# Optimization experiments

Hardware: AMD Instinct MI355X
Metric: run time of the kernel (lower is better)

Reference implementation:

```python
import jax, jax.numpy as jnp
import numpy as np

B, C, D_IN, E = 4000, 128, 9, 10          # nodes, channels, sum irrep dims (0e+1o+2e), elements
OUT_IRREPS = [(1, 8, 3), (3, 11, 4)]       # (d_out, k3 paths, k2 paths) for 0e and 1o; k1 = 1


def _sparse(key, shape, p=0.15):
    # mimic the sparse generalized Clebsch-Gordan (U-matrix) bases from e3nn
    k1, k2 = jax.random.split(key)
    vals = jax.random.normal(k1, shape, dtype=jnp.float32)
    mask = (jax.random.uniform(k2, shape) < p).astype(jnp.float32)
    return vals * mask


def setup_inputs() -> dict:
    key = jax.random.key(0)
    ks = jax.random.split(key, 20)
    x = jax.random.normal(ks[0], (B, C, D_IN), dtype=jnp.float32)
    elems = jax.random.randint(ks[1], (B,), 0, E)
    attrs = jax.nn.one_hot(elems, E, dtype=jnp.float32)  # one-hot element embedding
    inp = {"x": x, "attrs": attrs}
    i = 2
    for n, (d, k3, k2) in enumerate(OUT_IRREPS):
        inp[f"U3_{n}"] = _sparse(ks[i], (d, D_IN, D_IN, D_IN, k3)); i += 1
        inp[f"U2_{n}"] = _sparse(ks[i], (d, D_IN, D_IN, k2)); i += 1
        inp[f"U1_{n}"] = _sparse(ks[i], (d, D_IN, 1)); i += 1
        inp[f"W3_{n}"] = jax.random.normal(ks[i], (E, k3, C), dtype=jnp.float32) / k3; i += 1
        inp[f"W2_{n}"] = jax.random.normal(ks[i], (E, k2, C), dtype=jnp.float32) / k2; i += 1
        inp[f"W1_{n}"] = jax.random.normal(ks[i], (E, 1, C), dtype=jnp.float32); i += 1
    return inp


def _contract(x, attrs, U3, U2, U1, W3, W2, W1):
    # MACE Contraction.forward: highest correlation order, then recursive descent
    # out = einsum('...ik,ekc,bci,be->bc...', U3, W3, x, attrs)  expressed efficiently:
    w3 = jnp.einsum("ekc,be->bkc", W3, attrs)                 # per-node element-selected weights
    out = jnp.einsum("dijpk,bkc,bcp->bcdij", U3, w3, x)       # [b,c,d,i,j]
    w2 = jnp.einsum("ekc,be->bkc", W2, attrs)
    c2 = jnp.einsum("dijk,bkc->bcdij", U2, w2) + out
    out = jnp.einsum("bcdij,bcj->bcdi", c2, x)                # contract one index with x
    w1 = jnp.einsum("ekc,be->bkc", W1, attrs)
    c1 = jnp.einsum("dik,bkc->bcdi", U1, w1) + out
    out = jnp.einsum("bcdi,bci->bcd", c1, x)                  # [b,c,d_out]
    return out.reshape(out.shape[0], -1)                      # [b, c*d_out]


def reference(x, attrs, U3_0, U2_0, U1_0, W3_0, W2_0, W1_0,
              U3_1, U2_1, U1_1, W3_1, W2_1, W1_1):
    o0 = _contract(x, attrs, U3_0, U2_0, U1_0, W3_0, W2_0, W1_0)  # 0e output: [b, 128]
    o1 = _contract(x, attrs, U3_1, U2_1, U1_1, W3_1, W2_1, W1_1)  # 1o output: [b, 384]
    return jnp.concatenate([o0, o1], axis=-1)                     # [b, 512]
```

## Files before the change

kernel.cpp:

```cpp
#include <hip/hip_runtime.h>

#define B_NODES 4000
#define C_CH    128
#define E_ELEM  10
#define NT1 9
#define NT2 45
#define NT3 165
#define NT  219
#define DG  4


#define OFF_A3_0 0
#define OFF_A3_1 1320
#define OFF_A2_0 6765
#define OFF_A2_1 6900
#define OFF_A1_0 7440
#define OFF_A1_1 7449
#define A_TOTAL  7476
#define OFF_G_BYTES 32768

__device__ inline void decode3(int t, int& i, int& j, int& p) {
    int idx = 0;
    for (int a = 0; a < 9; a++)
        for (int b = a; b < 9; b++)
            for (int c = b; c < 9; c++) {
                if (idx == t) { i = a; j = b; p = c; return; }
                idx++;
            }
}

__device__ inline void decode2(int t, int& i, int& j) {
    int idx = 0;
    for (int a = 0; a < 9; a++)
        for (int b = a; b < 9; b++) {
            if (idx == t) { i = a; j = b; return; }
            idx++;
        }
}

__device__ inline float sum3(const float* U, int d, int K, int k, int i, int j, int p) {
    auto at = [&](int a, int b, int c) {
        return U[(((d * 9 + a) * 9 + b) * 9 + c) * K + k];
    };
    if (i == j && j == p) return at(i, i, i);
    if (i == j)           return at(i, i, p) + at(i, p, i) + at(p, i, i);
    if (j == p)           return at(i, j, j) + at(j, i, j) + at(j, j, i);
    return at(i, j, p) + at(i, p, j) + at(j, i, p) + at(j, p, i) + at(p, i, j) + at(p, j, i);
}

__device__ inline float sum2(const float* U, int d, int K, int k, int i, int j) {
    auto at = [&](int a, int b) { return U[((d * 9 + a) * 9 + b) * K + k]; };
    return (i == j) ? at(i, i) : (at(i, j) + at(j, i));
}

__device__ inline unsigned short f2bf(float f) {
    unsigned u = __float_as_uint(f);
    unsigned r = u + 0x7fffu + ((u >> 16) & 1u);
    return (unsigned short)(r >> 16);
}

__global__ void a_build(const float* __restrict__ U3_0, const float* __restrict__ U2_0,
                        const float* __restrict__ U1_0, const float* __restrict__ U3_1,
                        const float* __restrict__ U2_1, const float* __restrict__ U1_1,
                        float* __restrict__ ws) {
    int tid = blockIdx.x * blockDim.x + threadIdx.x;
    if (tid < 1320) {
        int t3 = tid / 8, k = tid % 8;
        int i, j, p; decode3(t3, i, j, p);
        ws[OFF_A3_0 + tid] = sum3(U3_0, 0, 8, k, i, j, p);
    } else if (tid < 1320 + 5445) {
        int r = tid - 1320;
        int d = r / (165 * 11); int r2 = r % (165 * 11);
        int t3 = r2 / 11, k = r2 % 11;
        int i, j, p; decode3(t3, i, j, p);
        ws[OFF_A3_1 + r] = sum3(U3_1, d, 11, k, i, j, p);
    } else if (tid < 6765 + 135) {
        int r = tid - 6765;
        int t2 = r / 3, k = r % 3;
        int i, j; decode2(t2, i, j);
        ws[OFF_A2_0 + r] = sum2(U2_0, 0, 3, k, i, j);
    } else if (tid < 6900 + 540) {
        int r = tid - 6900;
        int d = r / 180; int t2 = (r % 180) / 4; int k = r % 4;
        int i, j; decode2(t2, i, j);
        ws[OFF_A2_1 + r] = sum2(U2_1, d, 4, k, i, j);
    } else if (tid < 7440 + 9) {
        int i = tid - 7440;
        ws[OFF_A1_0 + i] = U1_0[i];
    } else if (tid < 7449 + 27) {
        int r = tid - 7449;
        ws[OFF_A1_1 + r] = U1_1[r];
    }
}

__global__ void g_build(const float* __restrict__ W3_0, const float* __restrict__ W2_0,
                        const float* __restrict__ W1_0, const float* __restrict__ W3_1,
                        const float* __restrict__ W2_1, const float* __restrict__ W1_1,
                        const float* __restrict__ ws, unsigned short* __restrict__ G) {
    int tid = blockIdx.x * blockDim.x + threadIdx.x;
    if (tid >= E_ELEM * NT * C_CH) return;
    int c = tid & (C_CH - 1);
    int r = tid >> 7;
    int t = r % NT;
    int e = r / NT;

    float g[4];
    if (t < NT1) {
        int i = t;
        float w0 = W1_0[e * C_CH + c];
        float w1 = W1_1[e * C_CH + c];
        g[0] = ws[OFF_A1_0 + i] * w0;
        for (int d = 0; d < 3; d++) g[1 + d] = ws[OFF_A1_1 + d * 9 + i] * w1;
    } else if (t < NT1 + NT2) {
        int t2 = t - NT1;
        float s = 0.f;
        for (int k = 0; k < 3; k++) s += ws[OFF_A2_0 + t2 * 3 + k] * W2_0[(e * 3 + k) * C_CH + c];
        g[0] = s;
        for (int d = 0; d < 3; d++) {
            s = 0.f;
            for (int k = 0; k < 4; k++) s += ws[OFF_A2_1 + (d * 45 + t2) * 4 + k] * W2_1[(e * 4 + k) * C_CH + c];
            g[1 + d] = s;
        }
    } else {
        int t3 = t - NT1 - NT2;
        float s = 0.f;
        for (int k = 0; k < 8; k++) s += ws[OFF_A3_0 + t3 * 8 + k] * W3_0[(e * 8 + k) * C_CH + c];
        g[0] = s;
        for (int d = 0; d < 3; d++) {
            s = 0.f;
            for (int k = 0; k < 11; k++) s += ws[OFF_A3_1 + (d * 165 + t3) * 11 + k] * W3_1[(e * 11 + k) * C_CH + c];
            g[1 + d] = s;
        }
    }
    uint2 u;
    u.x = (unsigned)f2bf(g[0]) | ((unsigned)f2bf(g[1]) << 16);
    u.y = (unsigned)f2bf(g[2]) | ((unsigned)f2bf(g[3]) << 16);
    reinterpret_cast<uint2*>(G)[tid] = u;
}

__global__ void __launch_bounds__(C_CH) sc_main(const float* __restrict__ x,
                                                const float* __restrict__ attrs,
                                                const unsigned short* __restrict__ G,
                                                float* __restrict__ out) {
    int b = blockIdx.x;
    int c = threadIdx.x;

    int e = 0;
#pragma unroll
    for (int q = 0; q < E_ELEM; q++) e += (attrs[b * E_ELEM + q] > 0.5f) ? q : 0;

    float y[9];
#pragma unroll
    for (int i = 0; i < 9; i++) y[i] = x[(b * C_CH + c) * 9 + i];

    float d2[45];
    {
        int q = 0;
#pragma unroll
        for (int i = 0; i < 9; i++)
#pragma unroll
            for (int j = i; j < 9; j++) { d2[q] = y[i] * y[j]; q++; }
    }

    const uint2* gp = reinterpret_cast<const uint2*>(G) + (e * NT * C_CH + c);
    float a0 = 0.f, a1 = 0.f, a2 = 0.f, a3 = 0.f;

#define FMA4(U, PHI)                                                        \
    do {                                                                    \
        float _p = (PHI);                                                   \
        a0 = fmaf(_p, __uint_as_float((U).x << 16), a0);                    \
        a1 = fmaf(_p, __uint_as_float((U).x & 0xffff0000u), a1);            \
        a2 = fmaf(_p, __uint_as_float((U).y << 16), a2);                    \
        a3 = fmaf(_p, __uint_as_float((U).y & 0xffff0000u), a3);            \
    } while (0)

    int t = 0;
#pragma unroll
    for (int i = 0; i < 9; i++) {
        uint2 u = gp[t * C_CH]; t++;
        FMA4(u, y[i]);
    }
    {
        int q = 0;
#pragma unroll
        for (int i = 0; i < 9; i++)
#pragma unroll
            for (int j = i; j < 9; j++) {
                uint2 u = gp[t * C_CH]; t++;
                FMA4(u, d2[q]);
                q++;
            }
    }
    {
        int q = 0;
#pragma unroll
        for (int i = 0; i < 9; i++)
#pragma unroll
            for (int j = i; j < 9; j++) {
#pragma unroll
                for (int p = j; p < 9; p++) {
                    uint2 u = gp[t * C_CH]; t++;
                    FMA4(u, d2[q] * y[p]);
                }
                q++;
            }
    }
#undef FMA4

    out[b * 512 + c] = a0;
    int o1 = b * 512 + 128 + 3 * c;
    out[o1 + 0] = a1;
    out[o1 + 1] = a2;
    out[o1 + 2] = a3;
}

extern "C" void kernel_launch(void* const* d_in, const int* in_sizes, int n_in,
                              void* d_out, int out_size, void* d_ws, size_t ws_size,
                              hipStream_t stream) {
    const float* x     = (const float*)d_in[0];
    const float* attrs = (const float*)d_in[1];
    const float* U3_0  = (const float*)d_in[2];
    const float* U2_0  = (const float*)d_in[3];
    const float* U1_0  = (const float*)d_in[4];
    const float* W3_0  = (const float*)d_in[5];
    const float* W2_0  = (const float*)d_in[6];
    const float* W1_0  = (const float*)d_in[7];
    const float* U3_1  = (const float*)d_in[8];
    const float* U2_1  = (const float*)d_in[9];
    const float* U1_1  = (const float*)d_in[10];
    const float* W3_1  = (const float*)d_in[11];
    const float* W2_1  = (const float*)d_in[12];
    const float* W1_1  = (const float*)d_in[13];

    float* wsA = (float*)d_ws;
    unsigned short* G = (unsigned short*)((char*)d_ws + OFF_G_BYTES);

    a_build<<<(A_TOTAL + 255) / 256, 256, 0, stream>>>(U3_0, U2_0, U1_0, U3_1, U2_1, U1_1, wsA);

    int ng = E_ELEM * NT * C_CH;
    g_build<<<(ng + 255) / 256, 256, 0, stream>>>(W3_0, W2_0, W1_0, W3_1, W2_1, W1_1, wsA, G);

    sc_main<<<B_NODES, C_CH, 0, stream>>>(x, attrs, G, (float*)d_out);
}
```

Before: 71.25 us.

## Pack monomial pairs as fp16 and accumulate with packed dot2 instructions

Repacks the precomputed per-element weight table G so that each uint4 holds fp16 pairs for two consecutive monomials across all four outputs. The main kernel then converts pairs of monomial products to fp16 and accumulates with fdot2, roughly halving the FMA instruction count. It also stages x through shared memory with coalesced float4 loads and sets an occupancy hint in launch bounds. The risk is lost accuracy: fp16 has limited range for cubic products of normal inputs, so values could overflow or lose precision compared with the previous bf16-weight/fp32-product scheme.

After: 59.21 us. 1.2x faster.

```diff
diff --git a/kernel.cpp b/kernel.cpp
--- a/kernel.cpp
+++ b/kernel.cpp
@@ -1,13 +1,13 @@
 #include <hip/hip_runtime.h>
+#include <utility>
+
+typedef _Float16 f16x2 __attribute__((ext_vector_type(2)));
 
 #define B_NODES 4000
 #define C_CH    128
 #define E_ELEM  10
-#define NT1 9
-#define NT2 45
-#define NT3 165
-#define NT  219
-#define DG  4
+#define NT      219
+#define NPAIR   110
 
 
 #define OFF_A3_0 0
@@ -19,6 +19,46 @@
 #define A_TOTAL  7476
 #define OFF_G_BYTES 32768
 
+#if defined(__has_builtin)
+#if __has_builtin(__builtin_amdgcn_fdot2)
+#define HAVE_FDOT2 1
+#endif
+#endif
+
+struct M3 { int i, j, p, deg; };
+
+constexpr M3 mono(int t) {
+    if (t < 9) return M3{t, 0, 0, 1};
+    int r = t - 9;
+    if (r < 45) {
+        int idx = 0;
+        for (int a = 0; a < 9; a++)
+            for (int b = a; b < 9; b++) {
+                if (idx == r) return M3{a, b, 0, 2};
+                idx++;
+            }
+    }
+    r -= 45;
+    {
+        int idx = 0;
+        for (int a = 0; a < 9; a++)
+            for (int b = a; b < 9; b++)
+                for (int c = b; c < 9; c++) {
+                    if (idx == r) return M3{a, b, c, 3};
+                    idx++;
+                }
+    }
+    return M3{0, 0, 0, 0};
+}
+
+template <int T>
+__device__ __forceinline__ float phi_t(const float (&y)[9]) {
+    constexpr M3 m = mono(T);
+    if constexpr (m.deg == 1) return y[m.i];
+    else if constexpr (m.deg == 2) return y[m.i] * y[m.j];
+    else return (y[m.i] * y[m.j]) * y[m.p];
+}
+
 __device__ inline void decode3(int t, int& i, int& j, int& p) {
     int idx = 0;
     for (int a = 0; a < 9; a++)
@@ -51,12 +91,6 @@
 __device__ inline float sum2(const float* U, int d, int K, int k, int i, int j) {
     auto at = [&](int a, int b) { return U[((d * 9 + a) * 9 + b) * K + k]; };
     return (i == j) ? at(i, i) : (at(i, j) + at(j, i));
-}
-
-__device__ inline unsigned short f2bf(float f) {
-    unsigned u = __float_as_uint(f);
-    unsigned r = u + 0x7fffu + ((u >> 16) & 1u);
-    return (unsigned short)(r >> 16);
 }
 
 __global__ void a_build(const float* __restrict__ U3_0, const float* __restrict__ U2_0,
@@ -93,26 +127,20 @@
     }
 }
 
-__global__ void g_build(const float* __restrict__ W3_0, const float* __restrict__ W2_0,
-                        const float* __restrict__ W1_0, const float* __restrict__ W3_1,
-                        const float* __restrict__ W2_1, const float* __restrict__ W1_1,
-                        const float* __restrict__ ws, unsigned short* __restrict__ G) {
-    int tid = blockIdx.x * blockDim.x + threadIdx.x;
-    if (tid >= E_ELEM * NT * C_CH) return;
-    int c = tid & (C_CH - 1);
-    int r = tid >> 7;
-    int t = r % NT;
-    int e = r / NT;
-
-    float g[4];
-    if (t < NT1) {
+__device__ void compute_g(int t, int e, int c, const float* __restrict__ ws,
+                          const float* __restrict__ W3_0, const float* __restrict__ W2_0,
+                          const float* __restrict__ W1_0, const float* __restrict__ W3_1,
+                          const float* __restrict__ W2_1, const float* __restrict__ W1_1,
+                          float g[4]) {
+    if (t >= NT) { g[0] = g[1] = g[2] = g[3] = 0.f; return; }
+    if (t < 9) {
         int i = t;
         float w0 = W1_0[e * C_CH + c];
         float w1 = W1_1[e * C_CH + c];
         g[0] = ws[OFF_A1_0 + i] * w0;
         for (int d = 0; d < 3; d++) g[1 + d] = ws[OFF_A1_1 + d * 9 + i] * w1;
-    } else if (t < NT1 + NT2) {
-        int t2 = t - NT1;
+    } else if (t < 9 + 45) {
+        int t2 = t - 9;
         float s = 0.f;
         for (int k = 0; k < 3; k++) s += ws[OFF_A2_0 + t2 * 3 + k] * W2_0[(e * 3 + k) * C_CH + c];
         g[0] = s;
@@ -122,7 +150,7 @@
             g[1 + d] = s;
         }
     } else {
-        int t3 = t - NT1 - NT2;
+        int t3 = t - 54;
         float s = 0.f;
         for (int k = 0; k < 8; k++) s += ws[OFF_A3_0 + t3 * 8 + k] * W3_0[(e * 8 + k) * C_CH + c];
         g[0] = s;
@@ -132,80 +160,98 @@
             g[1 + d] = s;
         }
     }
-    uint2 u;
-    u.x = (unsigned)f2bf(g[0]) | ((unsigned)f2bf(g[1]) << 16);
-    u.y = (unsigned)f2bf(g[2]) | ((unsigned)f2bf(g[3]) << 16);
-    reinterpret_cast<uint2*>(G)[tid] = u;
-}
-
-__global__ void __launch_bounds__(C_CH) sc_main(const float* __restrict__ x,
-                                                const float* __restrict__ attrs,
-                                                const unsigned short* __restrict__ G,
-                                                float* __restrict__ out) {
+}
+
+__device__ inline unsigned pack_h2(float a, float b) {
+    unsigned short ha = __builtin_bit_cast(unsigned short, (_Float16)a);
+    unsigned short hb = __builtin_bit_cast(unsigned short, (_Float16)b);
+    return (unsigned)ha | ((unsigned)hb << 16);
+}
+
+__global__ void g_build(const float* __restrict__ W3_0, const float* __restrict__ W2_0,
+                        const float* __restrict__ W1_0, const float* __restrict__ W3_1,
+                        const float* __restrict__ W2_1, const float* __restrict__ W1_1,
+                        const float* __restrict__ ws, uint4* __restrict__ G) {
+    int tid = blockIdx.x * blockDim.x + threadIdx.x;
+    if (tid >= E_ELEM * NPAIR * C_CH) return;
+    int c = tid & (C_CH - 1);
+    int r = tid >> 7;
+    int tp = r % NPAIR;
+    int e = r / NPAIR;
+
+    float ga[4], gb[4];
+    compute_g(2 * tp,     e, c, ws, W3_0, W2_0, W1_0, W3_1, W2_1, W1_1, ga);
+    compute_g(2 * tp + 1, e, c, ws, W3_0, W2_0, W1_0, W3_1, W2_1, W1_1, gb);
+
+    uint4 u;
+    u.x = pack_h2(ga[0], gb[0]);
+    u.y = pack_h2(ga[1], gb[1]);
+    u.z = pack_h2(ga[2], gb[2]);
+    u.w = pack_h2(ga[3], gb[3]);
+    G[tid] = u;
+}
+
+__device__ __forceinline__ float dot2acc(unsigned w, f16x2 p, float acc) {
+#ifdef HAVE_FDOT2
+    return __builtin_amdgcn_fdot2(__builtin_bit_cast(f16x2, w), p, acc, false);
+#else
+    f16x2 h = __builtin_bit_cast(f16x2, w);
+    return fmaf((float)p.x, (float)h.x, fmaf((float)p.y, (float)h.y, acc));
+#endif
+}
+
+template <int TP>
+__device__ __forceinline__ void pair_step(const float (&y)[9], const uint4* __restrict__ gp,
+                                          float& a0, float& a1, float& a2, float& a3) {
+    uint4 u = gp[TP * C_CH];
+    float p0 = phi_t<2 * TP>(y);
+    float p1 = 0.f;
+    if constexpr (2 * TP + 1 < NT) p1 = phi_t<2 * TP + 1>(y);
+    f16x2 p;
+    p.x = (_Float16)p0;
+    p.y = (_Float16)p1;
+    a0 = dot2acc(u.x, p, a0);
+    a1 = dot2acc(u.y, p, a1);
+    a2 = dot2acc(u.z, p, a2);
+    a3 = dot2acc(u.w, p, a3);
+}
+
+template <std::size_t... I>
+__device__ __forceinline__ void run_all(std::index_sequence<I...>, const float (&y)[9],
+                                        const uint4* __restrict__ gp,
+                                        float& a0, float& a1, float& a2, float& a3) {
+    (pair_step<(int)I>(y, gp, a0, a1, a2, a3), ...);
+}
+
+__global__ void __launch_bounds__(C_CH, 8) sc_main(const float* __restrict__ x,
+                                                   const float* __restrict__ attrs,
+                                                   const uint4* __restrict__ G,
+                                                   float* __restrict__ out) {
+    __shared__ __align__(16) float xs[C_CH * 9];
     int b = blockIdx.x;
     int c = threadIdx.x;
+
+    const float4* xsrc = reinterpret_cast<const float4*>(x + (size_t)b * C_CH * 9);
+    float4* xdst = reinterpret_cast<float4*>(xs);
+#pragma unroll
+    for (int k = 0; k < 3; k++) {
+        int idx = c + k * C_CH;
+        if (idx < 288) xdst[idx] = xsrc[idx];
+    }
 
     int e = 0;
 #pragma unroll
     for (int q = 0; q < E_ELEM; q++) e += (attrs[b * E_ELEM + q] > 0.5f) ? q : 0;
 
+    __syncthreads();
+
     float y[9];
 #pragma unroll
-    for (int i = 0; i < 9; i++) y[i] = x[(b * C_CH + c) * 9 + i];
-
-    float d2[45];
-    {
-        int q = 0;
-#pragma unroll
-        for (int i = 0; i < 9; i++)
-#pragma unroll
-            for (int j = i; j < 9; j++) { d2[q] = y[i] * y[j]; q++; }
-    }
-
-    const uint2* gp = reinterpret_cast<const uint2*>(G) + (e * NT * C_CH + c);
+    for (int i = 0; i < 9; i++) y[i] = xs[c * 9 + i];
+
     float a0 = 0.f, a1 = 0.f, a2 = 0.f, a3 = 0.f;
-
-#define FMA4(U, PHI)                                                        \
-    do {                                                                    \
-        float _p = (PHI);                                                   \
-        a0 = fmaf(_p, __uint_as_float((U).x << 16), a0);                    \
-        a1 = fmaf(_p, __uint_as_float((U).x & 0xffff0000u), a1);            \
-        a2 = fmaf(_p, __uint_as_float((U).y << 16), a2);                    \
-        a3 = fmaf(_p, __uint_as_float((U).y & 0xffff0000u), a3);            \
-    } while (0)
-
-    int t = 0;
-#pragma unroll
-    for (int i = 0; i < 9; i++) {
-        uint2 u = gp[t * C_CH]; t++;
-        FMA4(u, y[i]);
-    }
-    {
-        int q = 0;
-#pragma unroll
-        for (int i = 0; i < 9; i++)
-#pragma unroll
-            for (int j = i; j < 9; j++) {
-                uint2 u = gp[t * C_CH]; t++;
-                FMA4(u, d2[q]);
-                q++;
-            }
-    }
-    {
-        int q = 0;
-#pragma unroll
-        for (int i = 0; i < 9; i++)
-#pragma unroll
-            for (int j = i; j < 9; j++) {
-#pragma unroll
-                for (int p = j; p < 9; p++) {
-                    uint2 u = gp[t * C_CH]; t++;
-                    FMA4(u, d2[q] * y[p]);
-                }
-                q++;
-            }
-    }
-#undef FMA4
+    const uint4* gp = G + ((size_t)e * NPAIR * C_CH + c);
+    run_all(std::make_index_sequence<NPAIR>{}, y, gp, a0, a1, a2, a3);
 
     out[b * 512 + c] = a0;
     int o1 = b * 512 + 128 + 3 * c;
@@ -233,11 +279,11 @@
     const float* W1_1  = (const float*)d_in[13];
 
     float* wsA = (float*)d_ws;
-    unsigned short* G = (unsigned short*)((char*)d_ws + OFF_G_BYTES);
+    uint4* G = (uint4*)((char*)d_ws + OFF_G_BYTES);
 
     a_build<<<(A_TOTAL + 255) / 256, 256, 0, stream>>>(U3_0, U2_0, U1_0, U3_1, U2_1, U1_1, wsA);
 
-    int ng = E_ELEM * NT * C_CH;
+    int ng = E_ELEM * NPAIR * C_CH;
     g_build<<<(ng + 255) / 256, 256, 0, stream>>>(W3_0, W2_0, W1_0, W3_1, W2_1, W1_1, wsA, G);
 
     sc_main<<<B_NODES, C_CH, 0, stream>>>(x, attrs, G, (float*)d_out);
```
